# Kernel tuning notes

Measured on AMD Instinct MI355X. Metric: run time of the kernel, lower is better.

Reference implementation:

```python
import math
import jax, jax.numpy as jnp
import numpy as np

NUM_SPECIES = 4
RCR = 5.2
RCA = 3.5
ETA_R = 16.0
ETA_A = 8.0
ZETA = 32.0
SHFR = jnp.linspace(0.9, 5.2, 17)[:-1]                      # (16,) radial shifts
SHFA = jnp.linspace(0.9, 3.5, 5)[:-1]                       # (4,) angular dist shifts
SHFZ = jnp.linspace(0.0, math.pi, 9)[:-1] + math.pi / 16.0  # (8,) angle shifts
NUM_PAIRS = NUM_SPECIES * (NUM_SPECIES + 1) // 2            # 10 species pairs


def _triu_index(num_species):
    # symmetric map (s1, s2) -> index of unordered species pair (torchani get_triu_index)
    s1, s2 = np.triu_indices(num_species)
    ret = np.zeros((num_species, num_species), dtype=np.int32)
    ret[s1, s2] = np.arange(len(s1))
    ret[s2, s1] = np.arange(len(s1))
    return jnp.asarray(ret)

TRIU = _triu_index(NUM_SPECIES)


def _cutoff_cosine(d, rc):
    return 0.5 * jnp.cos(d * (math.pi / rc)) + 0.5


def _aev(species, coordinates):
    # species: (N,A) int, -1 = padding; coordinates: (N,A,3) float
    N, A = species.shape
    valid = species >= 0
    # diff[n,i,j] = r_i - r_j  (vector from neighbor j to atom i)
    diff = coordinates[:, :, None, :] - coordinates[:, None, :, :]   # (N,A,A,3)
    d2 = jnp.sum(diff * diff, axis=-1)                               # (N,A,A)
    eye = jnp.eye(A, dtype=bool)
    pair_ok = valid[:, :, None] & valid[:, None, :] & ~eye
    d = jnp.sqrt(jnp.where(d2 > 0, d2, 1.0))                         # safe norm (masked below)

    # ---------------- radial sub-AEV ----------------
    rmask = pair_ok & (d <= RCR)
    fc_r = _cutoff_cosine(d, RCR)
    rad = 0.25 * jnp.exp(-ETA_R * (d[..., None] - SHFR) ** 2) * fc_r[..., None]  # (N,A,A,16)
    rad = jnp.where(rmask[..., None], rad, 0.0)
    onehot_s = jax.nn.one_hot(species, NUM_SPECIES, dtype=rad.dtype)             # (N,A,S)
    radial_aev = jnp.einsum('nijf,njs->nisf', rad, onehot_s)                     # scatter-add by neighbor species
    radial_aev = radial_aev.reshape(N, A, NUM_SPECIES * SHFR.shape[0])           # (N,A,64)

    # ---------------- angular sub-AEV ----------------
    amask = pair_ok & (d <= RCA)                                     # neighbor within Rca of center
    jlk = jnp.triu(jnp.ones((A, A), dtype=bool), k=1)                # unordered pair j<k
    tmask = amask[:, :, :, None] & amask[:, :, None, :] & jlk[None, None]        # (N,A,A,A) [n,i,j,k]
    # angle at center i between (r_j - r_i) and (r_k - r_i): sign cancels using diff = r_i - r_j
    dot = jnp.einsum('nijc,nikc->nijk', diff, diff)                  # (N,A,A,A)
    denom = jnp.maximum(d[:, :, :, None] * d[:, :, None, :], 1e-10)
    angles = jnp.arccos(0.95 * (dot / denom))
    fcj = _cutoff_cosine(d, RCA)
    fc_prod = fcj[:, :, :, None] * fcj[:, :, None, :]
    dsum_half = 0.5 * (d[:, :, :, None] + d[:, :, None, :])
    factor1 = ((1.0 + jnp.cos(angles[..., None] - SHFZ)) * 0.5) ** ZETA          # (N,A,A,A,8)
    factor2 = jnp.exp(-ETA_A * (dsum_half[..., None] - SHFA) ** 2)               # (N,A,A,A,4)
    terms = 2.0 * factor2[..., :, None] * factor1[..., None, :] * fc_prod[..., None, None]  # (N,A,A,A,4,8)
    terms = jnp.where(tmask[..., None, None], terms, 0.0)
    terms = terms.reshape(N, A, A, A, SHFA.shape[0] * SHFZ.shape[0])             # (N,A,A,A,32), ShfA outer / ShfZ inner
    pair_idx = TRIU[species[:, :, None], species[:, None, :]]                    # (N,A,A)
    pair_onehot = jax.nn.one_hot(pair_idx, NUM_PAIRS, dtype=terms.dtype)         # (N,A,A,P)
    angular_aev = jnp.einsum('nijkf,njkp->nipf', terms, pair_onehot)             # scatter-add by species pair
    angular_aev = angular_aev.reshape(N, A, NUM_PAIRS * SHFA.shape[0] * SHFZ.shape[0])  # (N,A,320)

    return jnp.concatenate([radial_aev, angular_aev], axis=-1)      # (N,A,384)


def setup_inputs() -> dict:
    key = jax.random.key(0)
    k1, k2 = jax.random.split(key)
    N, A = 32, 48
    species = jax.random.randint(k1, (N, A), 0, NUM_SPECIES)
    # atoms uniformly placed in a 10 Angstrom box -> realistic mix of in/out-of-cutoff pairs
    coordinates = jax.random.uniform(k2, (N, A, 3), dtype=jnp.float32) * 10.0
    return {"species": species, "coordinates": coordinates}


def reference(species, coordinates):
    return _aev(species, coordinates)
```

## Files before the change

kernel.cpp:

```cpp
#include <hip/hip_runtime.h>
#include <math.h>

#define A_ATOMS 48
#define RADLEN  64
#define ANGLEN  320
#define FEATLEN 384
#define RCR_F 5.2f
#define RCA_F 3.5f

__device__ __constant__ float COSZ[8] = {
     0.98078528f,  0.83146961f,  0.55557023f,  0.19509032f,
    -0.19509032f, -0.55557023f, -0.83146961f, -0.98078528f};
__device__ __constant__ float SINZ[8] = {
     0.19509032f,  0.55557023f,  0.83146961f,  0.98078528f,
     0.98078528f,  0.83146961f,  0.55557023f,  0.19509032f};

__global__ __launch_bounds__(64) void aev_kernel(const int* __restrict__ species,
                                                 const float* __restrict__ coords,
                                                 float* __restrict__ out,
                                                 int N, int A) {
    const int blk = blockIdx.x;
    const int n = blk / A;
    const int i = blk - n * A;
    const int tid = threadIdx.x;

    __shared__ float sx[A_ATOMS], sy[A_ATOMS], szc[A_ATOMS];
    __shared__ int   sspec[A_ATOMS];
    __shared__ float ddx[A_ATOMS], ddy[A_ATOMS], ddz[A_ATOMS], dd[A_ATOMS];
    __shared__ float feat[FEATLEN];
    __shared__ int   nb_cnt;
    __shared__ int   nb_jj[A_ATOMS];
    __shared__ float nb_dx[A_ATOMS], nb_dy[A_ATOMS], nb_dz[A_ATOMS];
    __shared__ float nb_d[A_ATOMS], nb_fc[A_ATOMS];

    if (tid < A) {
        const float* c = coords + ((size_t)n * A + tid) * 3;
        sx[tid]  = c[0];
        sy[tid]  = c[1];
        szc[tid] = c[2];
        sspec[tid] = species[n * A + tid];
    }
    for (int t = tid; t < FEATLEN; t += 64) feat[t] = 0.f;
    if (tid == 0) nb_cnt = 0;
    __syncthreads();

    const int  si = sspec[i];
    const bool vi = (si >= 0);
    const float xi = sx[i], yi = sy[i], zi = szc[i];

    if (tid < A) {
        const int j = tid;
        float dx = 0.f, dy = 0.f, dz = 0.f, d = 1e30f;
        if (vi && j != i && sspec[j] >= 0) {
            dx = xi - sx[j]; dy = yi - sy[j]; dz = zi - szc[j];
            float d2 = dx*dx + dy*dy + dz*dz;
            d = (d2 > 0.f) ? sqrtf(d2) : 1.0f;
        }
        ddx[j] = dx; ddy[j] = dy; ddz[j] = dz; dd[j] = d;
        if (d <= RCA_F) {
            int slot = atomicAdd(&nb_cnt, 1);
            nb_jj[slot] = j;
            nb_dx[slot] = dx; nb_dy[slot] = dy; nb_dz[slot] = dz;
            nb_d[slot]  = d;
            nb_fc[slot] = 0.5f * __cosf(d * (float)(M_PI / 3.5)) + 0.5f;
        }
    }
    __syncthreads();

    if (tid < RADLEN) {
        const int s = tid >> 4;
        const int f = tid & 15;
        const float shfr = 0.9f + 0.26875f * (float)f;
        float acc = 0.f;
        for (int j = 0; j < A; ++j) {
            float d = dd[j];
            if (d <= RCR_F && sspec[j] == s) {
                float fc = 0.5f * __cosf(d * (float)(M_PI / 5.2)) + 0.5f;
                float e = d - shfr;
                acc += 0.25f * __expf(-16.f * e * e) * fc;
            }
        }
        feat[tid] = acc;
    }

    const int M = nb_cnt;
    const int P = (M * (M - 1)) >> 1;
    for (int p = tid; p < P; p += 64) {
        int a = (int)((1.f + sqrtf(1.f + 8.f * (float)p)) * 0.5f);
        while ((a * (a - 1)) / 2 > p) --a;
        while (((a + 1) * a) / 2 <= p) ++a;
        const int b = p - (a * (a - 1)) / 2;

        const float djx = nb_dx[a], djy = nb_dy[a], djz = nb_dz[a], dj = nb_d[a];
        const float dkx = nb_dx[b], dky = nb_dy[b], dkz = nb_dz[b], dk = nb_d[b];
        const float dotp = djx*dkx + djy*dky + djz*dkz;
        const float x  = 0.95f * dotp / fmaxf(dj * dk, 1e-10f);
        const float sn = sqrtf(fmaxf(0.f, 1.f - x * x));
        const float dh = 0.5f * (dj + dk);
        const int sj = sspec[nb_jj[a]];
        const int sk = sspec[nb_jj[b]];
        const int lo = (sj < sk) ? sj : sk;
        const int hi = (sj < sk) ? sk : sj;
        const int pidx = (lo * (9 - lo)) / 2 + (hi - lo);
        float* dst = &feat[RADLEN + pidx * 32];
        const float base = 2.f * nb_fc[a] * nb_fc[b];
        #pragma unroll
        for (int aa = 0; aa < 4; ++aa) {
            float e  = dh - (0.9f + 0.65f * (float)aa);
            float f2 = base * __expf(-8.f * e * e);
            #pragma unroll
            for (int zz = 0; zz < 8; ++zz) {
                float c = x * COSZ[zz] + sn * SINZ[zz];
                float t = 0.5f * (1.f + c);
                float t2 = t * t, t4 = t2 * t2, t8 = t4 * t4, t16 = t8 * t8;
                atomicAdd(&dst[aa * 8 + zz], f2 * (t16 * t16));
            }
        }
    }
    __syncthreads();

    float* o = out + (size_t)blk * FEATLEN;
    for (int t = tid; t < FEATLEN; t += 64) o[t] = feat[t];
}

extern "C" void kernel_launch(void* const* d_in, const int* in_sizes, int n_in,
                              void* d_out, int out_size, void* d_ws, size_t ws_size,
                              hipStream_t stream) {
    const int*   species = (const int*)d_in[0];
    const float* coords  = (const float*)d_in[1];
    float*       out     = (float*)d_out;
    const int NA = in_sizes[0];
    const int A  = A_ATOMS;
    const int N  = NA / A;
    aev_kernel<<<dim3(NA), dim3(64), 0, stream>>>(species, coords, out, N, A);
}
```

Baseline: 69.50 us.

## Replace shared-memory atomic scatter with per-thread feature ownership over staged pair batches

The angular term now stages neighbor-pair geometry into shared memory in batches of 128. Each thread owns up to three of the 320 angular features and accumulates them in registers, so the shared-memory atomicAdd scatter is gone. The radial term iterates over a compacted list of neighbors inside the radial cutoff instead of all atoms. The block grows to 128 threads and results are written straight to global memory. In exchange, every thread scans every pair and computes only where the species pair matches, so many lanes idle or diverge; exp is recomputed per feature; and a barrier is added per batch.

```diff
diff --git a/kernel.cpp b/kernel.cpp
--- a/kernel.cpp
+++ b/kernel.cpp
@@ -2,9 +2,9 @@
 #include <math.h>
 
 #define A_ATOMS 48
+#define BLK     128
 #define RADLEN  64
 #define ANGLEN  320
-#define FEATLEN 384
 #define RCR_F 5.2f
 #define RCA_F 3.5f
 
@@ -15,112 +15,142 @@
      0.19509032f,  0.55557023f,  0.83146961f,  0.98078528f,
      0.98078528f,  0.83146961f,  0.55557023f,  0.19509032f};
 
-__global__ __launch_bounds__(64) void aev_kernel(const int* __restrict__ species,
-                                                 const float* __restrict__ coords,
-                                                 float* __restrict__ out,
-                                                 int N, int A) {
+__global__ __launch_bounds__(BLK) void aev_kernel(const int* __restrict__ species,
+                                                  const float* __restrict__ coords,
+                                                  float* __restrict__ out) {
     const int blk = blockIdx.x;
-    const int n = blk / A;
-    const int i = blk - n * A;
+    const int n = blk / A_ATOMS;
+    const int i = blk - n * A_ATOMS;
     const int tid = threadIdx.x;
 
-    __shared__ float sx[A_ATOMS], sy[A_ATOMS], szc[A_ATOMS];
+    __shared__ float sx[A_ATOMS], sy[A_ATOMS], sz_[A_ATOMS];
     __shared__ int   sspec[A_ATOMS];
-    __shared__ float ddx[A_ATOMS], ddy[A_ATOMS], ddz[A_ATOMS], dd[A_ATOMS];
-    __shared__ float feat[FEATLEN];
-    __shared__ int   nb_cnt;
-    __shared__ int   nb_jj[A_ATOMS];
+    __shared__ int   rr_cnt, nb_cnt;
+    __shared__ float rr_d[A_ATOMS], rr_fc[A_ATOMS];
+    __shared__ int   rr_s[A_ATOMS];
     __shared__ float nb_dx[A_ATOMS], nb_dy[A_ATOMS], nb_dz[A_ATOMS];
     __shared__ float nb_d[A_ATOMS], nb_fc[A_ATOMS];
+    __shared__ int   nb_s[A_ATOMS];
+    __shared__ float pr_x[BLK], pr_sn[BLK], pr_dh[BLK], pr_b2[BLK];
+    __shared__ int   pr_pi[BLK];
 
-    if (tid < A) {
-        const float* c = coords + ((size_t)n * A + tid) * 3;
+    if (tid < A_ATOMS) {
+        const float* c = coords + ((size_t)n * A_ATOMS + tid) * 3;
         sx[tid]  = c[0];
         sy[tid]  = c[1];
-        szc[tid] = c[2];
-        sspec[tid] = species[n * A + tid];
+        sz_[tid] = c[2];
+        sspec[tid] = species[n * A_ATOMS + tid];
     }
-    for (int t = tid; t < FEATLEN; t += 64) feat[t] = 0.f;
-    if (tid == 0) nb_cnt = 0;
+    if (tid == 0) { rr_cnt = 0; nb_cnt = 0; }
     __syncthreads();
 
-    const int  si = sspec[i];
-    const bool vi = (si >= 0);
-    const float xi = sx[i], yi = sy[i], zi = szc[i];
+    const float xi = sx[i], yi = sy[i], zi = sz_[i];
+    const bool  vi = (sspec[i] >= 0);
 
-    if (tid < A) {
+    if (tid < A_ATOMS) {
         const int j = tid;
-        float dx = 0.f, dy = 0.f, dz = 0.f, d = 1e30f;
         if (vi && j != i && sspec[j] >= 0) {
-            dx = xi - sx[j]; dy = yi - sy[j]; dz = zi - szc[j];
+            float dx = xi - sx[j], dy = yi - sy[j], dz = zi - sz_[j];
             float d2 = dx*dx + dy*dy + dz*dz;
-            d = (d2 > 0.f) ? sqrtf(d2) : 1.0f;
-        }
-        ddx[j] = dx; ddy[j] = dy; ddz[j] = dz; dd[j] = d;
-        if (d <= RCA_F) {
-            int slot = atomicAdd(&nb_cnt, 1);
-            nb_jj[slot] = j;
-            nb_dx[slot] = dx; nb_dy[slot] = dy; nb_dz[slot] = dz;
-            nb_d[slot]  = d;
-            nb_fc[slot] = 0.5f * __cosf(d * (float)(M_PI / 3.5)) + 0.5f;
-        }
-    }
-    __syncthreads();
-
-    if (tid < RADLEN) {
-        const int s = tid >> 4;
-        const int f = tid & 15;
-        const float shfr = 0.9f + 0.26875f * (float)f;
-        float acc = 0.f;
-        for (int j = 0; j < A; ++j) {
-            float d = dd[j];
-            if (d <= RCR_F && sspec[j] == s) {
-                float fc = 0.5f * __cosf(d * (float)(M_PI / 5.2)) + 0.5f;
-                float e = d - shfr;
-                acc += 0.25f * __expf(-16.f * e * e) * fc;
+            float d  = (d2 > 0.f) ? sqrtf(d2) : 1.0f;
+            if (d <= RCR_F) {
+                int s = atomicAdd(&rr_cnt, 1);
+                rr_d[s]  = d;
+                rr_fc[s] = 0.25f * (0.5f * __cosf(d * (float)(M_PI / 5.2)) + 0.5f);
+                rr_s[s]  = sspec[j];
             }
-        }
-        feat[tid] = acc;
-    }
-
-    const int M = nb_cnt;
-    const int P = (M * (M - 1)) >> 1;
-    for (int p = tid; p < P; p += 64) {
-        int a = (int)((1.f + sqrtf(1.f + 8.f * (float)p)) * 0.5f);
-        while ((a * (a - 1)) / 2 > p) --a;
-        while (((a + 1) * a) / 2 <= p) ++a;
-        const int b = p - (a * (a - 1)) / 2;
-
-        const float djx = nb_dx[a], djy = nb_dy[a], djz = nb_dz[a], dj = nb_d[a];
-        const float dkx = nb_dx[b], dky = nb_dy[b], dkz = nb_dz[b], dk = nb_d[b];
-        const float dotp = djx*dkx + djy*dky + djz*dkz;
-        const float x  = 0.95f * dotp / fmaxf(dj * dk, 1e-10f);
-        const float sn = sqrtf(fmaxf(0.f, 1.f - x * x));
-        const float dh = 0.5f * (dj + dk);
-        const int sj = sspec[nb_jj[a]];
-        const int sk = sspec[nb_jj[b]];
-        const int lo = (sj < sk) ? sj : sk;
-        const int hi = (sj < sk) ? sk : sj;
-        const int pidx = (lo * (9 - lo)) / 2 + (hi - lo);
-        float* dst = &feat[RADLEN + pidx * 32];
-        const float base = 2.f * nb_fc[a] * nb_fc[b];
-        #pragma unroll
-        for (int aa = 0; aa < 4; ++aa) {
-            float e  = dh - (0.9f + 0.65f * (float)aa);
-            float f2 = base * __expf(-8.f * e * e);
-            #pragma unroll
-            for (int zz = 0; zz < 8; ++zz) {
-                float c = x * COSZ[zz] + sn * SINZ[zz];
-                float t = 0.5f * (1.f + c);
-                float t2 = t * t, t4 = t2 * t2, t8 = t4 * t4, t16 = t8 * t8;
-                atomicAdd(&dst[aa * 8 + zz], f2 * (t16 * t16));
+            if (d <= RCA_F) {
+                int s = atomicAdd(&nb_cnt, 1);
+                nb_dx[s] = dx; nb_dy[s] = dy; nb_dz[s] = dz;
+                nb_d[s]  = d;
+                nb_fc[s] = 0.5f * __cosf(d * (float)(M_PI / 3.5)) + 0.5f;
+                nb_s[s]  = sspec[j];
             }
         }
     }
     __syncthreads();
 
-    float* o = out + (size_t)blk * FEATLEN;
-    for (int t = tid; t < FEATLEN; t += 64) o[t] = feat[t];
+    float* o = out + (size_t)blk * (RADLEN + ANGLEN);
+
+    if (tid < RADLEN) {
+        const int   s    = tid >> 4;
+        const float shfr = 0.9f + 0.26875f * (float)(tid & 15);
+        float acc = 0.f;
+        const int Mr = rr_cnt;
+        for (int m = 0; m < Mr; ++m) {
+            if (rr_s[m] == s) {
+                float e = rr_d[m] - shfr;
+                acc += rr_fc[m] * __expf(-16.f * e * e);
+            }
+        }
+        o[tid] = acc;
+    }
+
+    float accf[3] = {0.f, 0.f, 0.f};
+    int   pik[3];
+    float czk[3], szk[3], shk[3];
+    #pragma unroll
+    for (int k = 0; k < 3; ++k) {
+        int f = tid * 3 + k;
+        if (f < ANGLEN) {
+            pik[k] = f >> 5;
+            int aa = (f >> 3) & 3, zz = f & 7;
+            czk[k] = COSZ[zz]; szk[k] = SINZ[zz];
+            shk[k] = 0.9f + 0.65f * (float)aa;
+        } else {
+            pik[k] = -1; czk[k] = 0.f; szk[k] = 0.f; shk[k] = 0.f;
+        }
+    }
+
+    const int M = nb_cnt;
+    const int P = (M * (M - 1)) >> 1;
+    for (int pb = 0; pb < P; pb += BLK) {
+        const int p = pb + tid;
+        if (p < P) {
+            int a = (int)((1.f + sqrtf(1.f + 8.f * (float)p)) * 0.5f);
+            while ((a * (a - 1)) / 2 > p) --a;
+            while (((a + 1) * a) / 2 <= p) ++a;
+            const int b = p - (a * (a - 1)) / 2;
+
+            const float dj = nb_d[a], dk = nb_d[b];
+            const float dotp = nb_dx[a]*nb_dx[b] + nb_dy[a]*nb_dy[b] + nb_dz[a]*nb_dz[b];
+            const float x  = 0.95f * dotp / fmaxf(dj * dk, 1e-10f);
+            pr_x[tid]  = x;
+            pr_sn[tid] = sqrtf(fmaxf(0.f, 1.f - x * x));
+            pr_dh[tid] = 0.5f * (dj + dk);
+            pr_b2[tid] = 2.f * nb_fc[a] * nb_fc[b];
+            const int sj = nb_s[a], sk = nb_s[b];
+            const int lo = (sj < sk) ? sj : sk;
+            const int hi = (sj < sk) ? sk : sj;
+            pr_pi[tid] = (lo * (9 - lo)) / 2 + (hi - lo);
+        }
+        __syncthreads();
+        const int cnt = (P - pb < BLK) ? (P - pb) : BLK;
+        for (int m = 0; m < cnt; ++m) {
+            const float x  = pr_x[m];
+            const float sn = pr_sn[m];
+            const float dh = pr_dh[m];
+            const float b2 = pr_b2[m];
+            const int   pi = pr_pi[m];
+            #pragma unroll
+            for (int k = 0; k < 3; ++k) {
+                if (pi == pik[k]) {
+                    float c = x * czk[k] + sn * szk[k];
+                    float t = 0.5f * (1.f + c);
+                    float t2 = t*t, t4 = t2*t2, t8 = t4*t4, t16 = t8*t8;
+                    float e = dh - shk[k];
+                    accf[k] += b2 * __expf(-8.f * e * e) * (t16 * t16);
+                }
+            }
+        }
+        __syncthreads();
+    }
+
+    #pragma unroll
+    for (int k = 0; k < 3; ++k) {
+        int f = tid * 3 + k;
+        if (f < ANGLEN) o[RADLEN + f] = accf[k];
+    }
 }
 
 extern "C" void kernel_launch(void* const* d_in, const int* in_sizes, int n_in,
@@ -130,7 +160,5 @@
     const float* coords  = (const float*)d_in[1];
     float*       out     = (float*)d_out;
     const int NA = in_sizes[0];
-    const int A  = A_ATOMS;
-    const int N  = NA / A;
-    aev_kernel<<<dim3(NA), dim3(64), 0, stream>>>(species, coords, out, N, A);
+    aev_kernel<<<dim3(NA), dim3(BLK), 0, stream>>>(species, coords, out);
 }
```

Result: slower. 77.21 us (+11.1%).
